# Kernel optimization log

Measured on AMD Instinct MI355X. Metric: run time of the kernel, lower is better.

The kernel has to match this reference:

```python
import jax, jax.numpy as jnp
import numpy as np

N, E, D = 10000, 160000, 512


def gcn_conv(x, src, dst, W, b):
    # GCNConv (PyG default): linear -> sym-normalized aggregation with self-loops -> +bias
    n = x.shape[0]
    h = x @ W  # [N, D]
    loop = jnp.arange(n)
    s = jnp.concatenate([src, loop])
    d = jnp.concatenate([dst, loop])
    deg = jax.ops.segment_sum(jnp.ones_like(d, dtype=h.dtype), d, num_segments=n)
    dinv = jnp.where(deg > 0, jax.lax.rsqrt(deg), 0.0)
    norm = dinv[s] * dinv[d]  # [E+N]
    msg = h[s] * norm[:, None]  # [E+N, D]
    out = jax.ops.segment_sum(msg, d, num_segments=n)
    return out + b


def gnn_embed(x, edge_index, Ws, bs):
    src, dst = edge_index[0], edge_index[1]
    h = x
    L = len(Ws)
    for i in range(L):
        h = gcn_conv(h, src, dst, Ws[i], bs[i])
        if i < L - 1:
            h = jax.nn.relu(h)
    return jnp.mean(h, axis=0).reshape(1, -1)  # [1, D]


def setup_inputs() -> dict:
    key = jax.random.key(0)
    ks = jax.random.split(key, 16)
    x1 = jax.random.normal(ks[0], (N, D), dtype=jnp.float32)
    x2 = jax.random.normal(ks[1], (N, D), dtype=jnp.float32)
    edge_index1 = jax.random.randint(ks[2], (2, E), 0, N, dtype=jnp.int64)
    edge_index2 = jax.random.randint(ks[3], (2, E), 0, N, dtype=jnp.int64)
    sc = 1.0 / np.sqrt(D)
    W1 = jax.random.normal(ks[4], (D, D), dtype=jnp.float32) * sc
    W2 = jax.random.normal(ks[5], (D, D), dtype=jnp.float32) * sc
    W3 = jax.random.normal(ks[6], (D, D), dtype=jnp.float32) * sc
    b1 = jnp.zeros((D,), jnp.float32)
    b2 = jnp.zeros((D,), jnp.float32)
    b3 = jnp.zeros((D,), jnp.float32)
    # FCL comparison head: concat(u1,u2) [1,2D] -> Linear(2D,D) -> ReLU -> Linear(D,1) -> sigmoid
    Wf1 = jax.random.normal(ks[7], (2 * D, D), dtype=jnp.float32) * (1.0 / np.sqrt(2 * D))
    bf1 = jnp.zeros((D,), jnp.float32)
    Wf2 = jax.random.normal(ks[8], (D, 1), dtype=jnp.float32) * sc
    bf2 = jnp.zeros((1,), jnp.float32)
    return dict(x1=x1, x2=x2, edge_index1=edge_index1, edge_index2=edge_index2,
                W1=W1, W2=W2, W3=W3, b1=b1, b2=b2, b3=b3,
                Wf1=Wf1, bf1=bf1, Wf2=Wf2, bf2=bf2)


def reference(x1, x2, edge_index1, edge_index2, W1, W2, W3, b1, b2, b3, Wf1, bf1, Wf2, bf2):
    Ws, bs = (W1, W2, W3), (b1, b2, b3)
    u1 = gnn_embed(x1, edge_index1, Ws, bs)  # [1, D]
    u2 = gnn_embed(x2, edge_index2, Ws, bs)  # [1, D]
    z = jnp.concatenate([u1, u2], axis=1)  # [1, 2D]
    h = jax.nn.relu(z @ Wf1 + bf1)
    score = jax.nn.sigmoid(h @ Wf2 + bf2)  # [1, 1]
    return score
```

## Files before the change

### kernel.cpp

```cpp
#include <hip/hip_runtime.h>
#include <math.h>

#define NN 10000
#define NE 160000
#define DD 512
#define MPAD 20096

typedef __attribute__((ext_vector_type(8))) short bf16x8;
typedef __attribute__((ext_vector_type(4))) float f32x4;
typedef __attribute__((ext_vector_type(8))) unsigned short u16x8;

__device__ __forceinline__ unsigned short f2bf(float f) {
    unsigned u = __float_as_uint(f);
    u += 0x7FFFu + ((u >> 16) & 1u);
    return (unsigned short)(u >> 16);
}
__device__ __forceinline__ float bf2f(unsigned short h) {
    return __uint_as_float(((unsigned)h) << 16);
}

#define GLOAD16(g, l) __builtin_amdgcn_global_load_lds( \
    (const __attribute__((address_space(1))) void*)(unsigned long long)(const void*)(g), \
    (__attribute__((address_space(3))) void*)(unsigned)(unsigned long long)(void*)(l), \
    16, 0, 0)

#define NB_CVTX 5024
#define NB_CNT  1250
#define NB_CVTW 3072
__global__ __launch_bounds__(256) void k_pre(const float* __restrict__ x1,
                                             const float* __restrict__ x2,
                                             unsigned short* __restrict__ xb,
                                             const int* __restrict__ e1,
                                             const int* __restrict__ e2,
                                             int* __restrict__ cnt,
                                             const float* __restrict__ W1,
                                             const float* __restrict__ W2,
                                             const float* __restrict__ W3,
                                             unsigned short* __restrict__ Wt) {
    int bid = blockIdx.x;
    int tid = threadIdx.x;
    if (bid < NB_CVTX) {
        long long i8 = ((long long)bid * 256 + tid) * 8;
        int row = (int)(i8 >> 9);
        int col = (int)(i8 & 511);
        u16x8 ov;
        if (row < 2 * NN) {
            const float* src = (row < NN) ? (x1 + (size_t)row * DD + col)
                                          : (x2 + (size_t)(row - NN) * DD + col);
            float4 f0 = ((const float4*)src)[0];
            float4 f1 = ((const float4*)src)[1];
            ov[0] = f2bf(f0.x); ov[1] = f2bf(f0.y); ov[2] = f2bf(f0.z); ov[3] = f2bf(f0.w);
            ov[4] = f2bf(f1.x); ov[5] = f2bf(f1.y); ov[6] = f2bf(f1.z); ov[7] = f2bf(f1.w);
        } else {
            #pragma unroll
            for (int j = 0; j < 8; ++j) ov[j] = 0;
        }
        *(u16x8*)(xb + i8) = ov;
    } else if (bid < NB_CVTX + NB_CNT) {
        int i = (bid - NB_CVTX) * 256 + tid;
        if (i < NE) {
            atomicAdd(&cnt[e1[NE + i]], 1);
        } else {
            int e = i - NE;
            atomicAdd(&cnt[NN + e2[NE + e]], 1);
        }
    } else {
        __shared__ float t[16][17];
        int b2 = bid - NB_CVTX - NB_CNT;
        int z = b2 >> 10;
        int rem = b2 & 1023;
        int n0 = (rem & 31) * 16;
        int k0 = (rem >> 5) * 16;
        const float* W = (z == 0) ? W1 : (z == 1) ? W2 : W3;
        unsigned short* o = Wt + (size_t)z * DD * DD;
        int tx = tid & 15, ty = tid >> 4;
        t[ty][tx] = W[(size_t)(k0 + ty) * DD + n0 + tx];
        __syncthreads();
        o[(size_t)(n0 + ty) * DD + k0 + tx] = f2bf(t[tx][ty]);
    }
}

__global__ void k_scan(const int* cnt, int* offs, float* dinv) {
    int g = blockIdx.x;
    const int* c = cnt + g * NN;
    int* o = offs + g * (NN + 1);
    __shared__ int sums[1024];
    int t = threadIdx.x;
    const int PER = 10;
    int base = t * PER;
    int vals[PER];
    int local = 0;
    #pragma unroll
    for (int j = 0; j < PER; ++j) {
        int idx = base + j;
        int v = (idx < NN) ? c[idx] : 0;
        vals[j] = v; local += v;
        if (idx < NN) dinv[g * NN + idx] = rsqrtf((float)(v + 1));
    }
    sums[t] = local;
    __syncthreads();
    for (int off = 1; off < 1024; off <<= 1) {
        int v = (t >= off) ? sums[t - off] : 0;
        __syncthreads();
        sums[t] += v;
        __syncthreads();
    }
    int prefix = (t > 0) ? sums[t - 1] : 0;
    #pragma unroll
    for (int j = 0; j < PER; ++j) {
        int idx = base + j;
        if (idx < NN) { o[idx] = prefix; prefix += vals[j]; }
    }
    if (t == 1023) o[NN] = sums[1023];
}

__global__ void k_fill(const int* e1, const int* e2, const int* offs,
                       int* cursor, int* adj) {
    int i = blockIdx.x * blockDim.x + threadIdx.x;
    if (i >= 2 * NE) return;
    int g = (i < NE) ? 0 : 1;
    int e = i - g * NE;
    const int* ei = g ? e2 : e1;
    int s = ei[e];
    int d = ei[NE + e];
    int pos = atomicAdd(&cursor[g * NN + d], 1);
    adj[g * NE + offs[g * (NN + 1) + d] + pos] = s;
}

__global__ __launch_bounds__(256) void k_gemm(const unsigned short* __restrict__ A,
                                              const unsigned short* __restrict__ Bt,
                                              unsigned short* __restrict__ C) {
    __shared__ bf16x8 As[1024];
    __shared__ bf16x8 Bs[1024];
    int tid = threadIdx.x;
    int lane = tid & 63;
    int wid = tid >> 6;
    int wr = wid >> 1, wc = wid & 1;

    int b = blockIdx.x;
    int xcd = b & 7;
    int idx = b >> 3;
    int start = (xcd < 4) ? xcd * 79 : 316 + (xcd - 4) * 78;
    int gi = start + idx;
    int rp = gi >> 2, cb = gi & 3;
    int row0 = rp * 128, col0 = cb * 128;

    const unsigned short* gA[4];
    const unsigned short* gB[4];
    bf16x8* lA[4];
    bf16x8* lB[4];
    #pragma unroll
    for (int j = 0; j < 4; ++j) {
        int t = j * 4 + wid;
        int row = 64 * (t & 1) + lane;
        int kb = t >> 1;
        gA[j] = A + (size_t)(row0 + row) * DD + kb * 8;
        gB[j] = Bt + (size_t)(col0 + row) * DD + kb * 8;
        lA[j] = &As[t * 64];
        lB[j] = &Bs[t * 64];
    }

    f32x4 acc[4][4];
    #pragma unroll
    for (int m = 0; m < 4; ++m)
        #pragma unroll
        for (int n = 0; n < 4; ++n)
            acc[m][n] = (f32x4){0.f, 0.f, 0.f, 0.f};

    for (int k0 = 0; k0 < DD; k0 += 64) {
        #pragma unroll
        for (int j = 0; j < 4; ++j) GLOAD16(gA[j], lA[j]);
        #pragma unroll
        for (int j = 0; j < 4; ++j) GLOAD16(gB[j], lB[j]);
        #pragma unroll
        for (int j = 0; j < 4; ++j) { gA[j] += 64; gB[j] += 64; }
        __syncthreads();
        #pragma unroll
        for (int kk = 0; kk < 2; ++kk) {
            bf16x8 af[4], bfr[4];
            #pragma unroll
            for (int m = 0; m < 4; ++m) {
                int kb = kk * 4 + (lane >> 4);
                af[m]  = As[kb * 128 + wr * 64 + m * 16 + (lane & 15)];
                bfr[m] = Bs[kb * 128 + wc * 64 + m * 16 + (lane & 15)];
            }
            #pragma unroll
            for (int m = 0; m < 4; ++m)
                #pragma unroll
                for (int n = 0; n < 4; ++n)
                    acc[m][n] = __builtin_amdgcn_mfma_f32_16x16x32_bf16(af[m], bfr[n], acc[m][n], 0, 0, 0);
        }
        __syncthreads();
    }

    #pragma unroll
    for (int m = 0; m < 4; ++m) {
        int rbase = row0 + wr * 64 + m * 16 + (lane >> 4) * 4;
        #pragma unroll
        for (int n = 0; n < 4; ++n) {
            int col = col0 + wc * 64 + n * 16 + (lane & 15);
            f32x4 v = acc[m][n];
            #pragma unroll
            for (int i = 0; i < 4; ++i)
                C[(size_t)(rbase + i) * DD + col] = f2bf(v[i]);
        }
    }
}

template <bool RELU>
__global__ __launch_bounds__(256) void k_aggc(const unsigned short* __restrict__ h,
                                              const int* __restrict__ adj,
                                              const int* __restrict__ offs,
                                              const float* __restrict__ dinv,
                                              const float* __restrict__ bias,
                                              unsigned short* __restrict__ out) {
    int bid = blockIdx.x;
    int combo = bid & 7;
    int nb = bid >> 3;
    int g = combo >> 2;
    int yc = combo & 3;
    int wid = threadIdx.x >> 6;
    int lane = threadIdx.x & 63;
    int sub = lane >> 4;
    int li = lane & 15;
    int v = nb * 16 + wid * 4 + sub;
    int c = yc * 128 + li * 8;
    int gbase = g * NN;
    const int* o = offs + g * (NN + 1);
    int beg = o[v], end = o[v + 1];
    const int* a = adj + g * NE;
    float dv = dinv[gbase + v];
    const unsigned short* hb = h + c;

    u16x8 hv = *(const u16x8*)(hb + (size_t)(gbase + v) * DD);
    float acc[8];
    #pragma unroll
    for (int j = 0; j < 8; ++j) acc[j] = bf2f(hv[j]) * dv;

    int e = beg;
    for (; e + 4 <= end; e += 4) {
        int s0 = a[e] + gbase, s1 = a[e + 1] + gbase;
        int s2 = a[e + 2] + gbase, s3 = a[e + 3] + gbase;
        u16x8 r0 = *(const u16x8*)(hb + (size_t)s0 * DD);
        u16x8 r1 = *(const u16x8*)(hb + (size_t)s1 * DD);
        u16x8 r2 = *(const u16x8*)(hb + (size_t)s2 * DD);
        u16x8 r3 = *(const u16x8*)(hb + (size_t)s3 * DD);
        float d0 = dinv[s0], d1 = dinv[s1], d2 = dinv[s2], d3 = dinv[s3];
        #pragma unroll
        for (int j = 0; j < 8; ++j) {
            acc[j] = fmaf(bf2f(r0[j]), d0, acc[j]);
            acc[j] = fmaf(bf2f(r1[j]), d1, acc[j]);
            acc[j] = fmaf(bf2f(r2[j]), d2, acc[j]);
            acc[j] = fmaf(bf2f(r3[j]), d3, acc[j]);
        }
    }
    for (; e < end; ++e) {
        int s = a[e] + gbase;
        float ds = dinv[s];
        u16x8 hs = *(const u16x8*)(hb + (size_t)s * DD);
        #pragma unroll
        for (int j = 0; j < 8; ++j) acc[j] = fmaf(bf2f(hs[j]), ds, acc[j]);
    }

    float4 b0 = ((const float4*)(bias + c))[0];
    float4 b1 = ((const float4*)(bias + c))[1];
    float bb[8] = {b0.x, b0.y, b0.z, b0.w, b1.x, b1.y, b1.z, b1.w};
    u16x8 ov;
    #pragma unroll
    for (int j = 0; j < 8; ++j) {
        float x = fmaf(acc[j], dv, bb[j]);
        if (RELU) x = fmaxf(x, 0.f);
        ov[j] = f2bf(x);
    }
    *(u16x8*)(out + (size_t)(gbase + v) * DD + c) = ov;
}

__global__ __launch_bounds__(256) void k_meanpart(const unsigned short* __restrict__ h,
                                                  float* __restrict__ u) {
    __shared__ float sm[4][DD];
    int g = blockIdx.y;
    int chunk = blockIdx.x;
    int wid = threadIdx.x >> 6;
    int lane = threadIdx.x & 63;
    int c = lane * 8;
    const int rows_per = (NN + 127) / 128;
    int r0 = chunk * rows_per;
    int r1 = min(r0 + rows_per, NN);
    float acc[8] = {0.f, 0.f, 0.f, 0.f, 0.f, 0.f, 0.f, 0.f};
    for (int r = r0 + wid; r < r1; r += 4) {
        u16x8 hv = *(const u16x8*)(h + (size_t)(g * NN + r) * DD + c);
        #pragma unroll
        for (int j = 0; j < 8; ++j) acc[j] += bf2f(hv[j]);
    }
    #pragma unroll
    for (int j = 0; j < 8; ++j) sm[wid][c + j] = acc[j];
    __syncthreads();
    if (wid == 0) {
        #pragma unroll
        for (int j = 0; j < 8; ++j) {
            float s = sm[0][c + j] + sm[1][c + j] + sm[2][c + j] + sm[3][c + j];
            atomicAdd(&u[g * DD + c + j], s);
        }
    }
}

__global__ void k_head1(const float* __restrict__ u, const float* __restrict__ Wf1,
                        float* __restrict__ hacc) {
    int t = threadIdx.x;
    int kb = blockIdx.x;
    const float inv = 1.0f / (float)NN;
    float acc = 0.f;
    for (int k = kb * 32; k < kb * 32 + 32; ++k) {
        float z = u[k] * inv;
        acc = fmaf(z, Wf1[(size_t)k * DD + t], acc);
    }
    atomicAdd(&hacc[t], acc);
}

__global__ void k_head2(const float* __restrict__ hacc, const float* __restrict__ bf1,
                        const float* __restrict__ Wf2, const float* __restrict__ bf2,
                        float* __restrict__ outp) {
    __shared__ float red[DD];
    int t = threadIdx.x;
    float hv = fmaxf(hacc[t] + bf1[t], 0.f);
    red[t] = hv * Wf2[t];
    __syncthreads();
    for (int s = DD / 2; s > 0; s >>= 1) {
        if (t < s) red[t] += red[t + s];
        __syncthreads();
    }
    if (t == 0) outp[0] = 1.f / (1.f + expf(-(red[0] + bf2[0])));
}

extern "C" void kernel_launch(void* const* d_in, const int* in_sizes, int n_in,
                              void* d_out, int out_size, void* d_ws, size_t ws_size,
                              hipStream_t stream) {
    const float* x1  = (const float*)d_in[0];
    const float* x2  = (const float*)d_in[1];
    const int*   e1  = (const int*)d_in[2];
    const int*   e2  = (const int*)d_in[3];
    const float* W1  = (const float*)d_in[4];
    const float* W2  = (const float*)d_in[5];
    const float* W3  = (const float*)d_in[6];
    const float* b1  = (const float*)d_in[7];
    const float* b2  = (const float*)d_in[8];
    const float* b3  = (const float*)d_in[9];
    const float* Wf1 = (const float*)d_in[10];
    const float* bf1 = (const float*)d_in[11];
    const float* Wf2 = (const float*)d_in[12];
    const float* bf2 = (const float*)d_in[13];
    float* outp = (float*)d_out;

    char* w = (char*)d_ws;
    unsigned short* xb = (unsigned short*)w; w += (size_t)MPAD * DD * 2;
    unsigned short* hG = (unsigned short*)w; w += (size_t)MPAD * DD * 2;
    unsigned short* hA = (unsigned short*)w; w += (size_t)MPAD * DD * 2;
    unsigned short* Wt = (unsigned short*)w; w += (size_t)3 * DD * DD * 2;
    int*   adj    = (int*)w;   w += 2 * NE * 4;
    int*   offs   = (int*)w;   w += 2 * (NN + 1) * 4 + 8;
    float* dinv   = (float*)w; w += 2 * NN * 4;
    char*  zbase  = w;
    int*   cnt    = (int*)w;   w += 2 * NN * 4;
    int*   cursor = (int*)w;   w += 2 * NN * 4;
    float* u      = (float*)w; w += 2 * DD * 4;
    float* hacc   = (float*)w; w += DD * 4;
    size_t zeroBytes = (size_t)(w - zbase);

    hipMemsetAsync(zbase, 0, zeroBytes, stream);
    k_pre<<<NB_CVTX + NB_CNT + NB_CVTW, 256, 0, stream>>>(x1, x2, xb, e1, e2, cnt,
                                                          W1, W2, W3, Wt);
    k_scan<<<2, 1024, 0, stream>>>(cnt, offs, dinv);
    k_fill<<<(2 * NE + 255) / 256, 256, 0, stream>>>(e1, e2, offs, cursor, adj);

    const int ggrid = (MPAD / 128) * (DD / 128);
    const int aggGrid = (NN / 16) * 8;

    k_gemm<<<ggrid, 256, 0, stream>>>(xb, Wt, hG);
    k_aggc<true><<<aggGrid, 256, 0, stream>>>(hG, adj, offs, dinv, b1, hA);
    k_gemm<<<ggrid, 256, 0, stream>>>(hA, Wt + (size_t)DD * DD, hG);
    k_aggc<true><<<aggGrid, 256, 0, stream>>>(hG, adj, offs, dinv, b2, hA);
    k_gemm<<<ggrid, 256, 0, stream>>>(hA, Wt + (size_t)2 * DD * DD, hG);
    k_aggc<false><<<aggGrid, 256, 0, stream>>>(hG, adj, offs, dinv, b3, hA);

    k_meanpart<<<dim3(128, 2), 256, 0, stream>>>(hA, u);
    k_head1<<<32, DD, 0, stream>>>(u, Wf1, hacc);
    k_head2<<<1, DD, 0, stream>>>(hacc, bf1, Wf2, bf2, outp);
}
```

Baseline: 281.9 us.

## Double-buffer GEMM LDS tiles and stage output through LDS for vector stores

Replaces the single-buffered 64-wide K loop in the bf16 MFMA GEMM with a ping-pong of two 32-wide K stages, so global-to-LDS loads for the next stage are issued while the current stage computes. The epilogue now writes accumulators into padded LDS and then emits coalesced 16-byte stores instead of scattered 2-byte global stores. This uses more shared memory (34 KB) and so may lower occupancy, and it keeps one barrier per half-stage.

```diff
diff --git a/kernel.cpp b/kernel.cpp
--- a/kernel.cpp
+++ b/kernel.cpp
@@ -130,8 +130,12 @@
 __global__ __launch_bounds__(256) void k_gemm(const unsigned short* __restrict__ A,
                                               const unsigned short* __restrict__ Bt,
                                               unsigned short* __restrict__ C) {
-    __shared__ bf16x8 As[1024];
-    __shared__ bf16x8 Bs[1024];
+    __shared__ char smem[34816];
+    bf16x8* A0 = (bf16x8*)smem;
+    bf16x8* B0 = (bf16x8*)(smem + 8192);
+    bf16x8* A1 = (bf16x8*)(smem + 16384);
+    bf16x8* B1 = (bf16x8*)(smem + 24576);
+
     int tid = threadIdx.x;
     int lane = tid & 63;
     int wid = tid >> 6;
@@ -145,20 +149,34 @@
     int rp = gi >> 2, cb = gi & 3;
     int row0 = rp * 128, col0 = cb * 128;
 
-    const unsigned short* gA[4];
-    const unsigned short* gB[4];
-    bf16x8* lA[4];
-    bf16x8* lB[4];
-    #pragma unroll
-    for (int j = 0; j < 4; ++j) {
-        int t = j * 4 + wid;
-        int row = 64 * (t & 1) + lane;
-        int kb = t >> 1;
-        gA[j] = A + (size_t)(row0 + row) * DD + kb * 8;
-        gB[j] = Bt + (size_t)(col0 + row) * DD + kb * 8;
-        lA[j] = &As[t * 64];
-        lB[j] = &Bs[t * 64];
-    }
+    int ch0 = wid * 64 + lane;
+    int ch1 = 256 + wid * 64 + lane;
+    const unsigned short* gA0 = A + (size_t)(row0 + (ch0 & 127)) * DD + (ch0 >> 7) * 8;
+    const unsigned short* gA1 = A + (size_t)(row0 + (ch1 & 127)) * DD + (ch1 >> 7) * 8;
+    const unsigned short* gB0 = Bt + (size_t)(col0 + (ch0 & 127)) * DD + (ch0 >> 7) * 8;
+    const unsigned short* gB1 = Bt + (size_t)(col0 + (ch1 & 127)) * DD + (ch1 >> 7) * 8;
+
+#define STAGE(Ad, Bd) do { \
+        GLOAD16(gA0, (Ad) + wid * 64); \
+        GLOAD16(gA1, (Ad) + 256 + wid * 64); \
+        GLOAD16(gB0, (Bd) + wid * 64); \
+        GLOAD16(gB1, (Bd) + 256 + wid * 64); \
+        gA0 += 32; gA1 += 32; gB0 += 32; gB1 += 32; \
+    } while (0)
+
+#define COMPUTE(As_, Bs_) do { \
+        bf16x8 af[4], bfr[4]; \
+        _Pragma("unroll") \
+        for (int m = 0; m < 4; ++m) { \
+            af[m]  = (As_)[(lane >> 4) * 128 + wr * 64 + m * 16 + (lane & 15)]; \
+            bfr[m] = (Bs_)[(lane >> 4) * 128 + wc * 64 + m * 16 + (lane & 15)]; \
+        } \
+        _Pragma("unroll") \
+        for (int m = 0; m < 4; ++m) \
+            _Pragma("unroll") \
+            for (int n = 0; n < 4; ++n) \
+                acc[m][n] = __builtin_amdgcn_mfma_f32_16x16x32_bf16(af[m], bfr[n], acc[m][n], 0, 0, 0); \
+    } while (0)
 
     f32x4 acc[4][4];
     #pragma unroll
@@ -167,43 +185,40 @@
         for (int n = 0; n < 4; ++n)
             acc[m][n] = (f32x4){0.f, 0.f, 0.f, 0.f};
 
-    for (int k0 = 0; k0 < DD; k0 += 64) {
-        #pragma unroll
-        for (int j = 0; j < 4; ++j) GLOAD16(gA[j], lA[j]);
-        #pragma unroll
-        for (int j = 0; j < 4; ++j) GLOAD16(gB[j], lB[j]);
-        #pragma unroll
-        for (int j = 0; j < 4; ++j) { gA[j] += 64; gB[j] += 64; }
-        __syncthreads();
-        #pragma unroll
-        for (int kk = 0; kk < 2; ++kk) {
-            bf16x8 af[4], bfr[4];
-            #pragma unroll
-            for (int m = 0; m < 4; ++m) {
-                int kb = kk * 4 + (lane >> 4);
-                af[m]  = As[kb * 128 + wr * 64 + m * 16 + (lane & 15)];
-                bfr[m] = Bs[kb * 128 + wc * 64 + m * 16 + (lane & 15)];
-            }
-            #pragma unroll
-            for (int m = 0; m < 4; ++m)
-                #pragma unroll
-                for (int n = 0; n < 4; ++n)
-                    acc[m][n] = __builtin_amdgcn_mfma_f32_16x16x32_bf16(af[m], bfr[n], acc[m][n], 0, 0, 0);
-        }
-        __syncthreads();
-    }
-
+    STAGE(A0, B0);
+    __syncthreads();
+    #pragma unroll
+    for (int p = 0; p < 8; ++p) {
+        STAGE(A1, B1);
+        COMPUTE(A0, B0);
+        __syncthreads();
+        if (p < 7) STAGE(A0, B0);
+        COMPUTE(A1, B1);
+        __syncthreads();
+    }
+#undef STAGE
+#undef COMPUTE
+
+    unsigned short* cs = (unsigned short*)smem;
     #pragma unroll
     for (int m = 0; m < 4; ++m) {
-        int rbase = row0 + wr * 64 + m * 16 + (lane >> 4) * 4;
+        int r = wr * 64 + m * 16 + (lane >> 4) * 4;
         #pragma unroll
         for (int n = 0; n < 4; ++n) {
-            int col = col0 + wc * 64 + n * 16 + (lane & 15);
+            int col = wc * 64 + n * 16 + (lane & 15);
             f32x4 v = acc[m][n];
             #pragma unroll
             for (int i = 0; i < 4; ++i)
-                C[(size_t)(rbase + i) * DD + col] = f2bf(v[i]);
+                cs[(r + i) * 136 + col] = f2bf(v[i]);
         }
+    }
+    __syncthreads();
+    #pragma unroll
+    for (int rr = 0; rr < 8; ++rr) {
+        int row = rr * 16 + (tid >> 4);
+        int col = (tid & 15) * 8;
+        u16x8 vv = *(const u16x8*)(cs + row * 136 + col);
+        *(u16x8*)(C + (size_t)(row0 + row) * DD + col0 + col) = vv;
     }
 }
 
```

Result: faster. 274.1 us (-2.8%).
